# Kernel optimization log

Hardware: AMD Instinct MI355X
Metric: run time of the kernel (lower is better)

The kernel has to match this reference:

```python
import jax, jax.numpy as jnp
import numpy as np

D_MODEL = 1024
NUM_HEADS = 16
HEAD_DIM = D_MODEL // NUM_HEADS  # 64
B, S = 4, 2048


def setup_inputs() -> dict:
    key = jax.random.key(0)
    ks = jax.random.split(key, 10)
    scale = 1.0 / np.sqrt(D_MODEL)
    x = jax.random.normal(ks[0], (B, S, D_MODEL), dtype=jnp.float32)
    # per-head projection weights stacked over the head axis (matches ModuleList of Linears)
    Wq = jax.random.normal(ks[1], (NUM_HEADS, D_MODEL, HEAD_DIM), dtype=jnp.float32) * scale
    bq = jax.random.normal(ks[2], (NUM_HEADS, HEAD_DIM), dtype=jnp.float32) * 0.01
    Wk = jax.random.normal(ks[3], (NUM_HEADS, D_MODEL, HEAD_DIM), dtype=jnp.float32) * scale
    bk = jax.random.normal(ks[4], (NUM_HEADS, HEAD_DIM), dtype=jnp.float32) * 0.01
    Wv = jax.random.normal(ks[5], (NUM_HEADS, D_MODEL, HEAD_DIM), dtype=jnp.float32) * scale
    bv = jax.random.normal(ks[6], (NUM_HEADS, HEAD_DIM), dtype=jnp.float32) * 0.01
    Wo = jax.random.normal(ks[7], (D_MODEL, D_MODEL), dtype=jnp.float32) * scale
    bo = jax.random.normal(ks[8], (D_MODEL,), dtype=jnp.float32) * 0.01
    return {"hidden_state": x, "Wq": Wq, "bq": bq, "Wk": Wk, "bk": bk,
            "Wv": Wv, "bv": bv, "Wo": Wo, "bo": bo}


def reference(hidden_state, Wq, bq, Wk, bk, Wv, bv, Wo, bo):
    # q,k,v: [B, H, S, E]
    q = jnp.einsum('bsd,hde->bhse', hidden_state, Wq) + bq[None, :, None, :]
    k = jnp.einsum('bsd,hde->bhse', hidden_state, Wk) + bk[None, :, None, :]
    v = jnp.einsum('bsd,hde->bhse', hidden_state, Wv) + bv[None, :, None, :]
    scores = jnp.einsum('bhse,bhte->bhst', q, k) / jnp.sqrt(jnp.asarray(HEAD_DIM, q.dtype))
    weights = jax.nn.softmax(scores, axis=-1)  # [B, H, S, S]
    attn = jnp.einsum('bhst,bhte->bhse', weights, v)  # [B, H, S, E]
    # concat heads along feature dim (head order preserved)
    attn = jnp.transpose(attn, (0, 2, 1, 3)).reshape(hidden_state.shape[0], hidden_state.shape[1], D_MODEL)
    return attn @ Wo + bo
```

## Files before the change

### kernel.cpp

```cpp
#include <hip/hip_runtime.h>

typedef __bf16 bf16x8 __attribute__((ext_vector_type(8)));
typedef float f32x4 __attribute__((ext_vector_type(4)));
typedef unsigned int u32x4 __attribute__((ext_vector_type(4)));
typedef unsigned int u32x2 __attribute__((ext_vector_type(2)));
typedef unsigned short u16x8 __attribute__((ext_vector_type(8)));

#define MFMA_BF16(a, b, c) __builtin_amdgcn_mfma_f32_16x16x32_bf16((a), (b), (c), 0, 0, 0)

#define QSCALE 0.18033688011112043f

__device__ __forceinline__ unsigned short f2bf(float f) {
    unsigned int u = __builtin_bit_cast(unsigned int, f);
    u += 0x7FFFu + ((u >> 16) & 1u);
    return (unsigned short)(u >> 16);
}

__device__ __forceinline__ unsigned int pack_bf16_rne(float a, float b) {
    unsigned int ua = __builtin_bit_cast(unsigned int, a);
    unsigned int ub = __builtin_bit_cast(unsigned int, b);
    ua += 0x7FFFu + ((ua >> 16) & 1u);
    ub += 0x7FFFu + ((ub >> 16) & 1u);
    return __builtin_amdgcn_perm(ub, ua, 0x07060302);
}

#if __has_builtin(__builtin_amdgcn_cvt_pk_bf16_f32)
typedef __bf16 bf16x2 __attribute__((ext_vector_type(2)));
__device__ __forceinline__ unsigned int pack_bf16(float a, float b) {
    return __builtin_bit_cast(unsigned int, __builtin_amdgcn_cvt_pk_bf16_f32(a, b));
}
#else
__device__ __forceinline__ unsigned int pack_bf16(float a, float b) {
    return pack_bf16_rne(a, b);
}
#endif

#if __has_builtin(__builtin_amdgcn_exp2f)
__device__ __forceinline__ float fast_exp2(float x) { return __builtin_amdgcn_exp2f(x); }
#else
__device__ __forceinline__ float fast_exp2(float x) { return exp2f(x); }
#endif

__device__ __forceinline__ bf16x8 ldfrag(const unsigned short* p) {
    return __builtin_bit_cast(bf16x8, *(const u32x4*)p);
}

typedef const __attribute__((address_space(1))) void* gas_t;
typedef __attribute__((address_space(3))) void* las_t;
__device__ __forceinline__ void dma16(const unsigned short* g, unsigned short* l) {
    __builtin_amdgcn_global_load_lds((gas_t)(const void*)g, (las_t)(void*)l, 16, 0, 0);
}

__device__ __forceinline__ void pipeline_barrier() {
    __builtin_amdgcn_s_waitcnt(0);
    __syncthreads();
}


__global__ void cvt_x_kernel(const float* __restrict__ in, unsigned short* __restrict__ out) {
    long long t = (long long)blockIdx.x * 256 + threadIdx.x;
    const f32x4* p = (const f32x4*)in + t * 2;
    f32x4 v0 = p[0], v1 = p[1];
    u16x8 o;
    o[0] = f2bf(v0[0]); o[1] = f2bf(v0[1]); o[2] = f2bf(v0[2]); o[3] = f2bf(v0[3]);
    o[4] = f2bf(v1[0]); o[5] = f2bf(v1[1]); o[6] = f2bf(v1[2]); o[7] = f2bf(v1[3]);
    *((u16x8*)out + t) = o;
}

__global__ void cvt_wqkvT_kernel(const float* __restrict__ Wq, const float* __restrict__ Wk,
                                 const float* __restrict__ Wv, unsigned short* __restrict__ WT) {
    int n = blockIdx.x * 256 + threadIdx.x;
    int d0 = blockIdx.y * 8;
    int proj = n >> 10, rem = n & 1023, h = rem >> 6, e = rem & 63;
    const float* W = (proj == 0) ? Wq : (proj == 1) ? Wk : Wv;
    const float* src = W + (size_t)h * 65536 + (size_t)d0 * 64 + e;
    u16x8 o;
#pragma unroll
    for (int j = 0; j < 8; j++) o[j] = f2bf(src[j * 64]);
    *(u16x8*)(WT + (size_t)n * 1024 + d0) = o;
}

__global__ void cvt_woT_kernel(const float* __restrict__ Wo, unsigned short* __restrict__ WoT) {
    int n = blockIdx.x * 256 + threadIdx.x;
    int d0 = blockIdx.y * 8;
    const float* src = Wo + (size_t)d0 * 1024 + n;
    u16x8 o;
#pragma unroll
    for (int j = 0; j < 8; j++) o[j] = f2bf(src[j * 1024]);
    *(u16x8*)(WoT + (size_t)n * 1024 + d0) = o;
}


__global__ __launch_bounds__(256) void gemm_qkv_kernel(
    const unsigned short* __restrict__ A, const unsigned short* __restrict__ BT,
    const float* __restrict__ bq, const float* __restrict__ bk, const float* __restrict__ bv,
    unsigned short* __restrict__ Qo, unsigned short* __restrict__ Ko, unsigned short* __restrict__ VTo) {
    __shared__ unsigned short As[2 * 128 * 32];
    __shared__ unsigned short Bs[2 * 128 * 32];
    const int tid = threadIdx.x;
    const int m0 = blockIdx.y * 128, n0 = blockIdx.x * 128;
    const int w = tid >> 6, lane = tid & 63, lr = lane & 15, quad = lane >> 4;
    const int wy = w >> 1, wx = w & 1;
    f32x4 acc[4][4];
#pragma unroll
    for (int i = 0; i < 4; i++)
#pragma unroll
        for (int j = 0; j < 4; j++) acc[i][j] = (f32x4){0.f, 0.f, 0.f, 0.f};
    const int drow = lane >> 2;
    const int dchunk = (lane & 3) ^ (drow & 3);
    const unsigned short* gA = A + (size_t)(m0 + w * 32 + drow) * 1024 + dchunk * 8;
    const unsigned short* gB = BT + (size_t)(n0 + w * 32 + drow) * 1024 + dchunk * 8;
    const int swav = (w * 32) * 32;
    const int fcol = (quad ^ (lr & 3)) * 8;
    dma16(gA, As + swav);
    dma16(gA + 16 * 1024, As + swav + 16 * 32);
    dma16(gB, Bs + swav);
    dma16(gB + 16 * 1024, Bs + swav + 16 * 32);
    for (int k0 = 0; k0 < 1024; k0 += 32) {
        const int cur = (k0 >> 5) & 1;
        const unsigned short* cA = As + cur * 4096;
        const unsigned short* cB = Bs + cur * 4096;
        pipeline_barrier();
        bf16x8 af[4], bfr[4];
#pragma unroll
        for (int i = 0; i < 4; i++) af[i] = ldfrag(cA + (wy * 64 + i * 16 + lr) * 32 + fcol);
#pragma unroll
        for (int j = 0; j < 4; j++) bfr[j] = ldfrag(cB + (wx * 64 + j * 16 + lr) * 32 + fcol);
        if (k0 + 32 < 1024) {
            const int nb = (cur ^ 1) * 4096 + swav;
            dma16(gA + k0 + 32, As + nb);
            dma16(gA + k0 + 32 + 16 * 1024, As + nb + 16 * 32);
            dma16(gB + k0 + 32, Bs + nb);
            dma16(gB + k0 + 32 + 16 * 1024, Bs + nb + 16 * 32);
        }
#pragma unroll
        for (int i = 0; i < 4; i++)
#pragma unroll
            for (int j = 0; j < 4; j++) acc[i][j] = MFMA_BF16(af[i], bfr[j], acc[i][j]);
    }
#pragma unroll
    for (int j = 0; j < 4; j++) {
        int n = n0 + wx * 64 + j * 16 + lr;
        int proj = n >> 10, rem = n & 1023, h = rem >> 6, e = rem & 63;
        if (proj == 2) {
            float bb = bv[rem];
#pragma unroll
            for (int i = 0; i < 4; i++) {
                int m = m0 + wy * 64 + i * 16 + quad * 4;
                int batch = m >> 11, s = m & 2047;
                u32x2 pk;
                pk[0] = pack_bf16_rne(acc[i][j][0] + bb, acc[i][j][1] + bb);
                pk[1] = pack_bf16_rne(acc[i][j][2] + bb, acc[i][j][3] + bb);
                *(u32x2*)(VTo + (((size_t)batch * 16 + h) * 64 + e) * 2048 + s) = pk;
            }
        } else {
            const float* bias = (proj == 0) ? bq : bk;
            unsigned short* dst = (proj == 0) ? Qo : Ko;
            float bb = bias[rem];
            float scl = (proj == 0) ? QSCALE : 1.0f;
#pragma unroll
            for (int i = 0; i < 4; i++) {
#pragma unroll
                for (int r = 0; r < 4; r++) {
                    int m = m0 + wy * 64 + i * 16 + quad * 4 + r;
                    int batch = m >> 11, s = m & 2047;
                    dst[(((size_t)batch * 16 + h) * 2048 + s) * 64 + e] = f2bf((acc[i][j][r] + bb) * scl);
                }
            }
        }
    }
}

__global__ __launch_bounds__(256) void gemm_out_kernel(
    const unsigned short* __restrict__ A, const unsigned short* __restrict__ BT,
    const float* __restrict__ bo, float* __restrict__ out) {
    __shared__ unsigned short As[2 * 128 * 32];
    __shared__ unsigned short Bs[2 * 128 * 32];
    const int tid = threadIdx.x;
    const int m0 = blockIdx.y * 128, n0 = blockIdx.x * 128;
    const int w = tid >> 6, lane = tid & 63, lr = lane & 15, quad = lane >> 4;
    const int wy = w >> 1, wx = w & 1;
    f32x4 acc[4][4];
#pragma unroll
    for (int i = 0; i < 4; i++)
#pragma unroll
        for (int j = 0; j < 4; j++) acc[i][j] = (f32x4){0.f, 0.f, 0.f, 0.f};
    const int drow = lane >> 2;
    const int dchunk = (lane & 3) ^ (drow & 3);
    const unsigned short* gA = A + (size_t)(m0 + w * 32 + drow) * 1024 + dchunk * 8;
    const unsigned short* gB = BT + (size_t)(n0 + w * 32 + drow) * 1024 + dchunk * 8;
    const int swav = (w * 32) * 32;
    const int fcol = (quad ^ (lr & 3)) * 8;
    dma16(gA, As + swav);
    dma16(gA + 16 * 1024, As + swav + 16 * 32);
    dma16(gB, Bs + swav);
    dma16(gB + 16 * 1024, Bs + swav + 16 * 32);
    for (int k0 = 0; k0 < 1024; k0 += 32) {
        const int cur = (k0 >> 5) & 1;
        const unsigned short* cA = As + cur * 4096;
        const unsigned short* cB = Bs + cur * 4096;
        pipeline_barrier();
        bf16x8 af[4], bfr[4];
#pragma unroll
        for (int i = 0; i < 4; i++) af[i] = ldfrag(cA + (wy * 64 + i * 16 + lr) * 32 + fcol);
#pragma unroll
        for (int j = 0; j < 4; j++) bfr[j] = ldfrag(cB + (wx * 64 + j * 16 + lr) * 32 + fcol);
        if (k0 + 32 < 1024) {
            const int nb = (cur ^ 1) * 4096 + swav;
            dma16(gA + k0 + 32, As + nb);
            dma16(gA + k0 + 32 + 16 * 1024, As + nb + 16 * 32);
            dma16(gB + k0 + 32, Bs + nb);
            dma16(gB + k0 + 32 + 16 * 1024, Bs + nb + 16 * 32);
        }
#pragma unroll
        for (int i = 0; i < 4; i++)
#pragma unroll
            for (int j = 0; j < 4; j++) acc[i][j] = MFMA_BF16(af[i], bfr[j], acc[i][j]);
    }
#pragma unroll
    for (int j = 0; j < 4; j++) {
        int n = n0 + wx * 64 + j * 16 + lr;
        float bb = bo[n];
#pragma unroll
        for (int i = 0; i < 4; i++) {
#pragma unroll
            for (int r = 0; r < 4; r++) {
                int m = m0 + wy * 64 + i * 16 + quad * 4 + r;
                out[(size_t)m * 1024 + n] = acc[i][j][r] + bb;
            }
        }
    }
}

#define ST 72
__global__ __launch_bounds__(256) void attn_fa_kernel(
    const unsigned short* __restrict__ Q, const unsigned short* __restrict__ K,
    const unsigned short* __restrict__ VT, unsigned short* __restrict__ Out) {
    __shared__ unsigned short Ks[2 * 64 * 64];
    __shared__ unsigned short Vs[2 * 64 * 64];
    __shared__ unsigned short Ps[128 * ST];
    const int bh = blockIdx.y;
    const int q0 = blockIdx.x * 128;
    const int tid = threadIdx.x;
    const int w = tid >> 6, lane = tid & 63, lr = lane & 15, quad = lane >> 4;
    const unsigned short* Qh = Q + (size_t)bh * 2048 * 64;
    const unsigned short* Kh = K + (size_t)bh * 2048 * 64;
    const unsigned short* Vh = VT + (size_t)bh * 64 * 2048;

    const int drow = lane >> 3;
    const int dchunk = (lane & 7) ^ drow;
    const unsigned short* gK = Kh + (size_t)(w * 16 + drow) * 64 + dchunk * 8;
    const unsigned short* gV = Vh + (size_t)(w * 16 + drow) * 2048 + dchunk * 8;
    const int swav = (w * 16) * 64;
    dma16(gK, Ks + swav);
    dma16(gK + 8 * 64, Ks + swav + 8 * 64);
    dma16(gV, Vs + swav);
    dma16(gV + 8 * 2048, Vs + swav + 8 * 64);

    {
        int r = tid >> 1, c = (tid & 1) * 32;
        const unsigned short* g = Qh + (size_t)(q0 + r) * 64 + c;
        unsigned short* s = Ps + r * ST + c;
        *(u32x4*)s = *(const u32x4*)g;
        *(u32x4*)(s + 8) = *(const u32x4*)(g + 8);
        *(u32x4*)(s + 16) = *(const u32x4*)(g + 16);
        *(u32x4*)(s + 24) = *(const u32x4*)(g + 24);
    }
    bf16x8 qb[2][2];
#pragma unroll
    for (int nt = 0; nt < 2; nt++)
#pragma unroll
        for (int kc = 0; kc < 2; kc++)
            qb[nt][kc] = ldfrag(Ps + (w * 32 + nt * 16 + lr) * ST + kc * 32 + quad * 8);

    f32x4 o[2][4];
#pragma unroll
    for (int i = 0; i < 2; i++)
#pragma unroll
        for (int j = 0; j < 4; j++) o[i][j] = (f32x4){0.f, 0.f, 0.f, 0.f};
    float lp[2] = {0.f, 0.f};

    for (int t0 = 0; t0 < 2048; t0 += 64) {
        const int cur = (t0 >> 6) & 1;
        const unsigned short* cK = Ks + cur * 4096;
        const unsigned short* cV = Vs + cur * 4096;
        pipeline_barrier();
        bf16x8 ka[2][4], vb[2][4];
#pragma unroll
        for (int kc = 0; kc < 2; kc++)
#pragma unroll
            for (int mt = 0; mt < 4; mt++) {
                int fc = ((kc * 4 + quad) ^ (lr & 7)) * 8;
                ka[kc][mt] = ldfrag(cK + (mt * 16 + lr) * 64 + fc);
                vb[kc][mt] = ldfrag(cV + (mt * 16 + lr) * 64 + fc);
            }
        if (t0 + 64 < 2048) {
            const int nb = (cur ^ 1) * 4096 + swav;
            dma16(gK + (size_t)(t0 + 64) * 64, Ks + nb);
            dma16(gK + (size_t)(t0 + 64) * 64 + 8 * 64, Ks + nb + 8 * 64);
            dma16(gV + t0 + 64, Vs + nb);
            dma16(gV + t0 + 64 + 8 * 2048, Vs + nb + 8 * 64);
        }

        f32x4 sc[4][2];
#pragma unroll
        for (int mt = 0; mt < 4; mt++) {
            sc[mt][0] = (f32x4){0.f, 0.f, 0.f, 0.f};
            sc[mt][1] = (f32x4){0.f, 0.f, 0.f, 0.f};
        }
#pragma unroll
        for (int kc = 0; kc < 2; kc++)
#pragma unroll
            for (int mt = 0; mt < 4; mt++) {
                sc[mt][0] = MFMA_BF16(ka[kc][mt], qb[0][kc], sc[mt][0]);
                sc[mt][1] = MFMA_BF16(ka[kc][mt], qb[1][kc], sc[mt][1]);
            }

#pragma unroll
        for (int nt = 0; nt < 2; nt++) {
            unsigned short* prow = Ps + (w * 32 + nt * 16 + lr) * ST + quad * 4;
#pragma unroll
            for (int mt = 0; mt < 4; mt++) {
                float p0 = fast_exp2(sc[mt][nt][0]);
                float p1 = fast_exp2(sc[mt][nt][1]);
                float p2 = fast_exp2(sc[mt][nt][2]);
                float p3 = fast_exp2(sc[mt][nt][3]);
                lp[nt] += (p0 + p1) + (p2 + p3);
                u32x2 pk;
                pk[0] = pack_bf16(p0, p1);
                pk[1] = pack_bf16(p2, p3);
                *(u32x2*)(prow + mt * 16) = pk;
            }
        }

#pragma unroll
        for (int kc = 0; kc < 2; kc++) {
            bf16x8 pa0 = ldfrag(Ps + (w * 32 + lr) * ST + kc * 32 + quad * 8);
            bf16x8 pa1 = ldfrag(Ps + (w * 32 + 16 + lr) * ST + kc * 32 + quad * 8);
#pragma unroll
            for (int et = 0; et < 4; et++) {
                o[0][et] = MFMA_BF16(pa0, vb[kc][et], o[0][et]);
                o[1][et] = MFMA_BF16(pa1, vb[kc][et], o[1][et]);
            }
        }
    }

#pragma unroll
    for (int nt = 0; nt < 2; nt++) {
        float l = lp[nt];
        l += __shfl_xor(l, 16, 64);
        l += __shfl_xor(l, 32, 64);
        lp[nt] = l;
    }

    const int h = bh & 15, b = bh >> 4;
#pragma unroll
    for (int mt = 0; mt < 2; mt++) {
#pragma unroll
        for (int r = 0; r < 4; r++) {
            float l = __shfl(lp[mt], quad * 4 + r, 16);
            float inv = 1.0f / l;
            int s = q0 + w * 32 + mt * 16 + quad * 4 + r;
#pragma unroll
            for (int et = 0; et < 4; et++) {
                int col = h * 64 + et * 16 + lr;
                Out[((size_t)(b * 2048 + s)) * 1024 + col] = f2bf(o[mt][et][r] * inv);
            }
        }
    }
}


extern "C" void kernel_launch(void* const* d_in, const int* in_sizes, int n_in,
                              void* d_out, int out_size, void* d_ws, size_t ws_size,
                              hipStream_t stream) {
    const float* x  = (const float*)d_in[0];
    const float* Wq = (const float*)d_in[1];
    const float* bq = (const float*)d_in[2];
    const float* Wk = (const float*)d_in[3];
    const float* bk = (const float*)d_in[4];
    const float* Wv = (const float*)d_in[5];
    const float* bv = (const float*)d_in[6];
    const float* Wo = (const float*)d_in[7];
    const float* bo = (const float*)d_in[8];
    float* out = (float*)d_out;

    char* ws = (char*)d_ws;
    unsigned short* xb    = (unsigned short*)(ws);
    unsigned short* WqkvT = (unsigned short*)(ws + 16777216);
    unsigned short* WoT   = (unsigned short*)(ws + 23068672);
    unsigned short* Qb    = (unsigned short*)(ws + 25165824);
    unsigned short* Kb    = (unsigned short*)(ws + 41943040);
    unsigned short* VTb   = (unsigned short*)(ws + 58720256);
    unsigned short* attn  = xb;

    cvt_x_kernel<<<dim3(4096), dim3(256), 0, stream>>>(x, xb);
    cvt_wqkvT_kernel<<<dim3(12, 128), dim3(256), 0, stream>>>(Wq, Wk, Wv, WqkvT);
    cvt_woT_kernel<<<dim3(4, 128), dim3(256), 0, stream>>>(Wo, WoT);
    gemm_qkv_kernel<<<dim3(24, 64), dim3(256), 0, stream>>>(xb, WqkvT, bq, bk, bv, Qb, Kb, VTb);
    attn_fa_kernel<<<dim3(16, 64), dim3(256), 0, stream>>>(Qb, Kb, VTb, attn);
    gemm_out_kernel<<<dim3(8, 64), dim3(256), 0, stream>>>(attn, WoT, bo, out);
}
```

Measured before the change: 296.3 us.

## Load K/V fragments directly from global in attention, 256 queries per block

Measured after the change: 345.9 us. +16.7%, slower.

```diff
diff --git a/kernel.cpp b/kernel.cpp
--- a/kernel.cpp
+++ b/kernel.cpp
@@ -38,7 +38,11 @@
 #if __has_builtin(__builtin_amdgcn_exp2f)
 __device__ __forceinline__ float fast_exp2(float x) { return __builtin_amdgcn_exp2f(x); }
 #else
-__device__ __forceinline__ float fast_exp2(float x) { return exp2f(x); }
+__device__ __forceinline__ float fast_exp2(float x) {
+    float r;
+    asm("v_exp_f32 %0, %1\n\ts_nop 0" : "=v"(r) : "v"(x));
+    return r;
+}
 #endif
 
 __device__ __forceinline__ bf16x8 ldfrag(const unsigned short* p) {
@@ -116,6 +120,7 @@
     dma16(gA + 16 * 1024, As + swav + 16 * 32);
     dma16(gB, Bs + swav);
     dma16(gB + 16 * 1024, Bs + swav + 16 * 32);
+#pragma unroll 2
     for (int k0 = 0; k0 < 1024; k0 += 32) {
         const int cur = (k0 >> 5) & 1;
         const unsigned short* cA = As + cur * 4096;
@@ -195,6 +200,7 @@
     dma16(gA + 16 * 1024, As + swav + 16 * 32);
     dma16(gB, Bs + swav);
     dma16(gB + 16 * 1024, Bs + swav + 16 * 32);
+#pragma unroll 2
     for (int k0 = 0; k0 < 1024; k0 += 32) {
         const int cur = (k0 >> 5) & 1;
         const unsigned short* cA = As + cur * 4096;
@@ -233,92 +239,73 @@
 }
 
 #define ST 72
-__global__ __launch_bounds__(256) void attn_fa_kernel(
+__global__ __launch_bounds__(256, 2) void attn_fa_kernel(
     const unsigned short* __restrict__ Q, const unsigned short* __restrict__ K,
     const unsigned short* __restrict__ VT, unsigned short* __restrict__ Out) {
-    __shared__ unsigned short Ks[2 * 64 * 64];
-    __shared__ unsigned short Vs[2 * 64 * 64];
-    __shared__ unsigned short Ps[128 * ST];
-    const int bh = blockIdx.y;
-    const int q0 = blockIdx.x * 128;
+    __shared__ unsigned short Ps[256 * ST];
+    const int bh = blockIdx.x;
+    const int q0 = blockIdx.y * 256;
     const int tid = threadIdx.x;
     const int w = tid >> 6, lane = tid & 63, lr = lane & 15, quad = lane >> 4;
+    const int W = w * 64;
     const unsigned short* Qh = Q + (size_t)bh * 2048 * 64;
     const unsigned short* Kh = K + (size_t)bh * 2048 * 64;
     const unsigned short* Vh = VT + (size_t)bh * 64 * 2048;
 
-    const int drow = lane >> 3;
-    const int dchunk = (lane & 7) ^ drow;
-    const unsigned short* gK = Kh + (size_t)(w * 16 + drow) * 64 + dchunk * 8;
-    const unsigned short* gV = Vh + (size_t)(w * 16 + drow) * 2048 + dchunk * 8;
-    const int swav = (w * 16) * 64;
-    dma16(gK, Ks + swav);
-    dma16(gK + 8 * 64, Ks + swav + 8 * 64);
-    dma16(gV, Vs + swav);
-    dma16(gV + 8 * 2048, Vs + swav + 8 * 64);
-
     {
-        int r = tid >> 1, c = (tid & 1) * 32;
-        const unsigned short* g = Qh + (size_t)(q0 + r) * 64 + c;
-        unsigned short* s = Ps + r * ST + c;
-        *(u32x4*)s = *(const u32x4*)g;
-        *(u32x4*)(s + 8) = *(const u32x4*)(g + 8);
-        *(u32x4*)(s + 16) = *(const u32x4*)(g + 16);
-        *(u32x4*)(s + 24) = *(const u32x4*)(g + 24);
-    }
-    bf16x8 qb[2][2];
-#pragma unroll
-    for (int nt = 0; nt < 2; nt++)
+        const unsigned short* g = Qh + (size_t)(q0 + W + lane) * 64;
+        unsigned short* s = Ps + (W + lane) * ST;
+#pragma unroll
+        for (int c = 0; c < 8; c++) *(u32x4*)(s + c * 8) = *(const u32x4*)(g + c * 8);
+    }
+    bf16x8 qb[4][2];
+#pragma unroll
+    for (int nt = 0; nt < 4; nt++)
 #pragma unroll
         for (int kc = 0; kc < 2; kc++)
-            qb[nt][kc] = ldfrag(Ps + (w * 32 + nt * 16 + lr) * ST + kc * 32 + quad * 8);
-
-    f32x4 o[2][4];
-#pragma unroll
-    for (int i = 0; i < 2; i++)
+            qb[nt][kc] = ldfrag(Ps + (W + nt * 16 + lr) * ST + kc * 32 + quad * 8);
+
+    f32x4 o[4][4];
+#pragma unroll
+    for (int i = 0; i < 4; i++)
 #pragma unroll
         for (int j = 0; j < 4; j++) o[i][j] = (f32x4){0.f, 0.f, 0.f, 0.f};
-    float lp[2] = {0.f, 0.f};
+    float lp[4] = {0.f, 0.f, 0.f, 0.f};
+
+    const unsigned short* gK = Kh + (size_t)lr * 64 + quad * 8;
+    const unsigned short* gV = Vh + (size_t)lr * 2048 + quad * 8;
 
     for (int t0 = 0; t0 < 2048; t0 += 64) {
-        const int cur = (t0 >> 6) & 1;
-        const unsigned short* cK = Ks + cur * 4096;
-        const unsigned short* cV = Vs + cur * 4096;
-        pipeline_barrier();
-        bf16x8 ka[2][4], vb[2][4];
+        bf16x8 ka[2][4];
 #pragma unroll
         for (int kc = 0; kc < 2; kc++)
 #pragma unroll
-            for (int mt = 0; mt < 4; mt++) {
-                int fc = ((kc * 4 + quad) ^ (lr & 7)) * 8;
-                ka[kc][mt] = ldfrag(cK + (mt * 16 + lr) * 64 + fc);
-                vb[kc][mt] = ldfrag(cV + (mt * 16 + lr) * 64 + fc);
-            }
-        if (t0 + 64 < 2048) {
-            const int nb = (cur ^ 1) * 4096 + swav;
-            dma16(gK + (size_t)(t0 + 64) * 64, Ks + nb);
-            dma16(gK + (size_t)(t0 + 64) * 64 + 8 * 64, Ks + nb + 8 * 64);
-            dma16(gV + t0 + 64, Vs + nb);
-            dma16(gV + t0 + 64 + 8 * 2048, Vs + nb + 8 * 64);
-        }
-
-        f32x4 sc[4][2];
-#pragma unroll
-        for (int mt = 0; mt < 4; mt++) {
-            sc[mt][0] = (f32x4){0.f, 0.f, 0.f, 0.f};
-            sc[mt][1] = (f32x4){0.f, 0.f, 0.f, 0.f};
-        }
+            for (int mt = 0; mt < 4; mt++)
+                ka[kc][mt] = ldfrag(gK + (size_t)(t0 + mt * 16) * 64 + kc * 32);
+
+        f32x4 sc[4][4];
+#pragma unroll
+        for (int mt = 0; mt < 4; mt++)
+#pragma unroll
+            for (int nt = 0; nt < 4; nt++) sc[mt][nt] = (f32x4){0.f, 0.f, 0.f, 0.f};
 #pragma unroll
         for (int kc = 0; kc < 2; kc++)
 #pragma unroll
-            for (int mt = 0; mt < 4; mt++) {
-                sc[mt][0] = MFMA_BF16(ka[kc][mt], qb[0][kc], sc[mt][0]);
-                sc[mt][1] = MFMA_BF16(ka[kc][mt], qb[1][kc], sc[mt][1]);
-            }
-
-#pragma unroll
-        for (int nt = 0; nt < 2; nt++) {
-            unsigned short* prow = Ps + (w * 32 + nt * 16 + lr) * ST + quad * 4;
+            for (int mt = 0; mt < 4; mt++)
+#pragma unroll
+                for (int nt = 0; nt < 4; nt++)
+                    sc[mt][nt] = MFMA_BF16(ka[kc][mt], qb[nt][kc], sc[mt][nt]);
+
+        bf16x8 vb[2][4];
+#pragma unroll
+        for (int kc = 0; kc < 2; kc++)
+#pragma unroll
+            for (int et = 0; et < 4; et++)
+                vb[kc][et] = ldfrag(gV + (size_t)(et * 16) * 2048 + t0 + kc * 32);
+
+#pragma unroll
+        for (int nt = 0; nt < 4; nt++) {
+            unsigned short* prow = Ps + (W + nt * 16 + lr) * ST + quad * 4;
 #pragma unroll
             for (int mt = 0; mt < 4; mt++) {
                 float p0 = fast_exp2(sc[mt][nt][0]);
@@ -335,18 +322,20 @@
 
 #pragma unroll
         for (int kc = 0; kc < 2; kc++) {
-            bf16x8 pa0 = ldfrag(Ps + (w * 32 + lr) * ST + kc * 32 + quad * 8);
-            bf16x8 pa1 = ldfrag(Ps + (w * 32 + 16 + lr) * ST + kc * 32 + quad * 8);
-#pragma unroll
-            for (int et = 0; et < 4; et++) {
-                o[0][et] = MFMA_BF16(pa0, vb[kc][et], o[0][et]);
-                o[1][et] = MFMA_BF16(pa1, vb[kc][et], o[1][et]);
-            }
-        }
-    }
-
-#pragma unroll
-    for (int nt = 0; nt < 2; nt++) {
+            bf16x8 pa[4];
+#pragma unroll
+            for (int nt = 0; nt < 4; nt++)
+                pa[nt] = ldfrag(Ps + (W + nt * 16 + lr) * ST + kc * 32 + quad * 8);
+#pragma unroll
+            for (int nt = 0; nt < 4; nt++)
+#pragma unroll
+                for (int et = 0; et < 4; et++)
+                    o[nt][et] = MFMA_BF16(pa[nt], vb[kc][et], o[nt][et]);
+        }
+    }
+
+#pragma unroll
+    for (int nt = 0; nt < 4; nt++) {
         float l = lp[nt];
         l += __shfl_xor(l, 16, 64);
         l += __shfl_xor(l, 32, 64);
@@ -355,16 +344,16 @@
 
     const int h = bh & 15, b = bh >> 4;
 #pragma unroll
-    for (int mt = 0; mt < 2; mt++) {
+    for (int nt = 0; nt < 4; nt++) {
 #pragma unroll
         for (int r = 0; r < 4; r++) {
-            float l = __shfl(lp[mt], quad * 4 + r, 16);
+            float l = __shfl(lp[nt], quad * 4 + r, 16);
             float inv = 1.0f / l;
-            int s = q0 + w * 32 + mt * 16 + quad * 4 + r;
+            int s = q0 + W + nt * 16 + quad * 4 + r;
 #pragma unroll
             for (int et = 0; et < 4; et++) {
                 int col = h * 64 + et * 16 + lr;
-                Out[((size_t)(b * 2048 + s)) * 1024 + col] = f2bf(o[mt][et][r] * inv);
+                Out[((size_t)(b * 2048 + s)) * 1024 + col] = f2bf(o[nt][et][r] * inv);
             }
         }
     }
@@ -398,6 +387,6 @@
     cvt_wqkvT_kernel<<<dim3(12, 128), dim3(256), 0, stream>>>(Wq, Wk, Wv, WqkvT);
     cvt_woT_kernel<<<dim3(4, 128), dim3(256), 0, stream>>>(Wo, WoT);
     gemm_qkv_kernel<<<dim3(24, 64), dim3(256), 0, stream>>>(xb, WqkvT, bq, bk, bv, Qb, Kb, VTb);
-    attn_fa_kernel<<<dim3(16, 64), dim3(256), 0, stream>>>(Qb, Kb, VTb, attn);
+    attn_fa_kernel<<<dim3(64, 8), dim3(256), 0, stream>>>(Qb, Kb, VTb, attn);
     gemm_out_kernel<<<dim3(8, 64), dim3(256), 0, stream>>>(attn, WoT, bo, out);
 }
```
